# Kernel optimization log

Measured on AMD Instinct MI355X. Metric: run time of the kernel, lower is better.

The kernel has to match this reference:

```python
import jax, jax.numpy as jnp
import numpy as np

B, S, D, HW = 256, 32, 512, 196


def setup_inputs() -> dict:
    key = jax.random.key(0)
    ks = jax.random.split(key, 34)
    n = lambda k, sh, s=1.0: jax.random.normal(k, sh, dtype=jnp.float32) * s
    w = 0.03  # xavier-ish scale for D=512 layers
    return {
        "words": n(ks[0], (B, S, D)),
        "question": n(ks[1], (B, 2 * D)),
        "know": n(ks[2], (B, D, HW)),
        "control0": n(ks[3], (B, D)),
        "memory0": n(ks[4], (B, D)),
        # ControlUnit
        "Wsc": n(ks[5], (2 * D, D), w), "bsc": jnp.zeros((D,), jnp.float32),
        "Wp": n(ks[6], (D, D), w), "bp": jnp.zeros((D,), jnp.float32),
        "Wcq": n(ks[7], (2 * D, D), w), "bcq": jnp.zeros((D,), jnp.float32),
        "wac": n(ks[8], (D, 1), w), "bac": jnp.zeros((1,), jnp.float32),
        # ReadUnit
        "Wm": n(ks[9], (D, D), w), "bm": jnp.zeros((D,), jnp.float32),
        "Wk": n(ks[10], (D, D), w), "bk": jnp.zeros((D,), jnp.float32),
        "Wc1": n(ks[11], (3 * D, D), w), "bc1": jnp.zeros((D,), jnp.float32),
        "Wc2": n(ks[12], (D, D), w), "bc2": jnp.zeros((D,), jnp.float32),
        "war": n(ks[13], (D, 1), w), "bar": jnp.zeros((1,), jnp.float32),
        # WriteUnit (self-attention variant)
        "Wwc": n(ks[14], (D, D), w), "bwc": jnp.zeros((D,), jnp.float32),
        "waw": n(ks[15], (D, 1), w), "baw": jnp.zeros((1,), jnp.float32),
        "Wwcat": n(ks[16], (3 * D, D), w), "bwcat": jnp.zeros((D,), jnp.float32),
    }


def reference(words, question, know, control0, memory0,
              Wsc, bsc, Wp, bp, Wcq, bcq, wac, bac,
              Wm, bm, Wk, bk, Wc1, bc1, Wc2, bc2, war, bar,
              Wwc, bwc, waw, baw, Wwcat, bwcat):
    # ---- ControlUnit (step 0) ----
    q = jnp.tanh(question @ Wsc + bsc)                    # [B,D]
    pa = q @ Wp + bp                                      # position_aware[0]
    cq = jnp.concatenate([control0, pa], axis=1) @ Wcq + bcq  # [B,D]
    logit_c = (cq[:, None, :] * words) @ wac + bac        # [B,S,1]
    attn_c = jax.nn.softmax(logit_c, axis=1)
    control = jnp.sum(attn_c * words, axis=1)             # [B,D]

    # ---- ReadUnit ----
    pm = memory0 @ Wm + bm                                # [B,D]
    pk = jnp.einsum('bdn,de->ben', know, Wk) + bk[None, :, None]  # [B,D,HW]
    pm_b = jnp.broadcast_to(pm[:, :, None], pk.shape)
    feat = jnp.concatenate([pm_b * pk, pk, pm_b], axis=1)  # [B,3D,HW]
    h = jax.nn.relu(jnp.einsum('bfn,fd->bnd', feat, Wc1) + bc1)  # [B,HW,D]
    h = h @ Wc2 + bc2                                     # [B,HW,D]
    logit_r = (h * control[:, None, :]) @ war + bar       # [B,HW,1]
    a_r = jax.nn.softmax(logit_r[..., 0], axis=1)          # [B,HW]
    read = jnp.einsum('bdn,bn->bd', know, a_r)            # [B,D]

    # ---- WriteUnit (self-attention over previous controls; T=1 at step 0) ----
    sc = control @ Wwc + bwc                              # [B,D]
    ctrl_prev = control0[:, :, None]                      # [B,D,T]
    logit_w = jnp.einsum('bdt,d->bt', sc[:, :, None] * ctrl_prev, waw[:, 0]) + baw  # [B,T]
    a_w = jax.nn.softmax(logit_w, axis=1)
    attn_mem = jnp.einsum('bdt,bt->bd', memory0[:, :, None], a_w)  # [B,D]
    concat = jnp.concatenate([read, memory0, attn_mem], axis=1)    # [B,3D]
    next_mem = concat @ Wwcat + bwcat                     # [B,D]

    return control, next_mem
```

## Files before the change

kernel.cpp:

```cpp
#include <hip/hip_runtime.h>
#include <hip/hip_bf16.h>
#include <math.h>

typedef __hip_bfloat16 bf16;
typedef __attribute__((ext_vector_type(8))) short s8v;
typedef __attribute__((ext_vector_type(4))) short s4v;
typedef __attribute__((ext_vector_type(4))) float f4v;

#define BB 256
#define SS 32
#define DD 512
#define HWN 196
#define AP 40

__device__ __forceinline__ float b2f(bf16 x){ return __bfloat162float(x); }
__device__ __forceinline__ bf16 f2b(float x){ return __float2bfloat16(x); }
__device__ __forceinline__ float us2f(unsigned short u){
    union { unsigned int i; float f; } t; t.i = ((unsigned int)u) << 16; return t.f;
}
__device__ __forceinline__ float ldin(int dt, const void* p, size_t i){
    return dt ? b2f(((const bf16*)p)[i]) : ((const float*)p)[i];
}

__global__ void detect_k(const void* q, int* flag){
    __shared__ int cnt;
    if (threadIdx.x == 0) cnt = 0;
    __syncthreads();
    const unsigned short* u = (const unsigned short*)q;
    unsigned short v = u[threadIdx.x * 4];
    int e = (v >> 7) & 0xFF;
    atomicAdd(&cnt, (e >= 100 && e <= 140) ? 1 : 0);
    __syncthreads();
    if (threadIdx.x == 0) *flag = (cnt > 128) ? 1 : 0;
}

struct PJob { const void* s; const void* s_b; const void* s2; const void* s2_b;
              bf16* d; int R, C, ldd, kofs, mode, boff; };
struct PrepP { PJob j[11]; const void* war; const void* bk; float* warf; float* bkf; };

__global__ __launch_bounds__(256) void prep_k(PrepP P, const int* __restrict__ flag){
    const int dt = *flag;
    __shared__ float T[32][33];
    int bx = blockIdx.x;
    int ji = 0;
    #pragma unroll
    for (int i = 0; i < 11; ++i) if (bx >= P.j[i].boff) ji = i;
    PJob jb = P.j[ji];
    const void* src  = dt ? jb.s_b  : jb.s;
    const void* src2 = dt ? jb.s2_b : jb.s2;
    int t = bx - jb.boff;
    int tx = threadIdx.x & 31, ty = threadIdx.x >> 5;
    if (jb.mode == 3){
        for (int i = threadIdx.x; i < DD; i += 256){
            P.warf[i] = ldin(dt, P.war, i);
            P.bkf[i]  = ldin(dt, P.bk, i);
        }
        return;
    }
    int nrt = jb.R >> 5;
    int r0 = (t % nrt) << 5, c0 = (t / nrt) << 5;
    if (jb.mode == 2){
        for (int rr = ty; rr < 32; rr += 8)
            jb.d[(size_t)(r0 + rr) * jb.ldd + jb.kofs + c0 + tx] =
                f2b(ldin(dt, src, (size_t)(r0 + rr) * jb.C + c0 + tx));
        return;
    }
    for (int rr = ty; rr < 32; rr += 8){
        float v = ldin(dt, src, (size_t)(r0 + rr) * jb.C + c0 + tx);
        if (jb.mode == 1) v += ldin(dt, src2, (size_t)(r0 + rr) * jb.C + c0 + tx);
        T[rr][tx] = v;
    }
    __syncthreads();
    for (int rr = ty; rr < 32; rr += 8)
        jb.d[(size_t)(c0 + rr) * jb.ldd + jb.kofs + r0 + tx] = f2b(T[tx][rr]);
}

__device__ __forceinline__ void tile_decode(int idb, int swz, int& rt, int& ct){
    if (swz){ int g = idb >> 6, w = idb & 63; rt = g * 8 + (w & 7); ct = w >> 3; }
    else    { ct = idb & 7; rt = idb >> 3; }
}

__global__ __launch_bounds__(256) void g1_mfma(const void* __restrict__ know,
                                               const bf16* __restrict__ BT,
                                               const float* __restrict__ bkf,
                                               bf16* __restrict__ C,
                                               int b0, int swz,
                                               const int* __restrict__ flag){
    const int dt = *flag;
    __shared__ __align__(16) bf16 As[128 * AP];
    __shared__ __align__(16) bf16 Bs[64 * AP];
    const int tid = threadIdx.x, lane = tid & 63, wave = tid >> 6;
    const int q = lane >> 4, mr = lane & 15;
    int rt, ct; tile_decode(blockIdx.x, swz, rt, ct);
    const int r0 = rt * 128, c0 = ct * 64;
    const int quad = tid >> 3;
    const int kg   = tid & 7;
    const int m    = r0 + quad * 4;
    const int bl   = m / HWN;
    const int n    = m - bl * HWN;
    const size_t abase = ((size_t)(b0 + bl) * DD) * HWN + n;
    f4v acc[2][4];
    #pragma unroll
    for (int t = 0; t < 2; ++t)
        #pragma unroll
        for (int j = 0; j < 4; ++j){ f4v z = {0.f,0.f,0.f,0.f}; acc[t][j] = z; }
    for (int k0 = 0; k0 < DD; k0 += 32){
        union { bf16 h[4]; s4v v; } pk_[4];
        if (dt == 0){
            const float* kp = (const float*)know + abase + (size_t)(k0 + kg * 4) * HWN;
            float4 ra = *(const float4*)kp;
            float4 rb = *(const float4*)(kp + HWN);
            float4 rc = *(const float4*)(kp + 2 * HWN);
            float4 rd4 = *(const float4*)(kp + 3 * HWN);
            #pragma unroll
            for (int j = 0; j < 4; ++j){
                pk_[j].h[0] = f2b((&ra.x)[j]);
                pk_[j].h[1] = f2b((&rb.x)[j]);
                pk_[j].h[2] = f2b((&rc.x)[j]);
                pk_[j].h[3] = f2b((&rd4.x)[j]);
            }
        } else {
            const unsigned short* kp = (const unsigned short*)know + abase + (size_t)(k0 + kg * 4) * HWN;
            ushort4 ua = *(const ushort4*)kp;
            ushort4 ub = *(const ushort4*)(kp + HWN);
            ushort4 uc = *(const ushort4*)(kp + 2 * HWN);
            ushort4 ud = *(const ushort4*)(kp + 3 * HWN);
            #pragma unroll
            for (int j = 0; j < 4; ++j){
                ((unsigned short*)&pk_[j].v)[0] = (&ua.x)[j];
                ((unsigned short*)&pk_[j].v)[1] = (&ub.x)[j];
                ((unsigned short*)&pk_[j].v)[2] = (&uc.x)[j];
                ((unsigned short*)&pk_[j].v)[3] = (&ud.x)[j];
            }
        }
        #pragma unroll
        for (int j = 0; j < 4; ++j)
            *(s4v*)&As[(quad * 4 + j) * AP + kg * 4] = pk_[j].v;
        {
            int col = tid >> 2, ko = (tid & 3) * 8;
            *(float4*)&Bs[col * AP + ko] =
                *(const float4*)(BT + (size_t)(c0 + col) * DD + k0 + ko);
        }
        __syncthreads();
        s8v a0 = *(const s8v*)&As[(wave * 32 + mr) * AP + q * 8];
        s8v a1 = *(const s8v*)&As[(wave * 32 + 16 + mr) * AP + q * 8];
        #pragma unroll
        for (int j = 0; j < 4; ++j){
            s8v b = *(const s8v*)&Bs[(j * 16 + mr) * AP + q * 8];
            acc[0][j] = __builtin_amdgcn_mfma_f32_16x16x32_bf16(a0, b, acc[0][j], 0, 0, 0);
            acc[1][j] = __builtin_amdgcn_mfma_f32_16x16x32_bf16(a1, b, acc[1][j], 0, 0, 0);
        }
        __syncthreads();
    }
    #pragma unroll
    for (int t = 0; t < 2; ++t)
        #pragma unroll
        for (int j = 0; j < 4; ++j)
            #pragma unroll
            for (int i = 0; i < 4; ++i){
                int row = r0 + wave * 32 + t * 16 + q * 4 + i;
                int col = c0 + j * 16 + mr;
                C[(size_t)row * DD + col] = f2b(acc[t][j][i] + bkf[col]);
            }
}

__global__ __launch_bounds__(256) void g2_mfma(const bf16* __restrict__ Apk,
                                               const bf16* __restrict__ BT,
                                               const float* __restrict__ pmf,
                                               const float* __restrict__ t3b,
                                               const float* __restrict__ uf,
                                               float* __restrict__ lpart,
                                               int b0, int swz){
    __shared__ __align__(16) bf16 As[128 * AP];
    __shared__ __align__(16) bf16 Bs[64 * AP];
    const int tid = threadIdx.x, lane = tid & 63, wave = tid >> 6;
    const int q = lane >> 4, mr = lane & 15;
    int idb = blockIdx.x, u, ct;
    if (swz){ int g = idb >> 6, w = idb & 63; u = g * 8 + (w & 7); ct = w >> 3; }
    else    { u = idb >> 3; ct = idb & 7; }
    const int bl = u >> 1, rt = u & 1;
    const int b = b0 + bl;
    const int c0 = ct * 64, rbase = rt * 128;
    const float* pmb = pmf + (size_t)b * DD;
    f4v acc[2][4];
    #pragma unroll
    for (int t = 0; t < 2; ++t)
        #pragma unroll
        for (int j = 0; j < 4; ++j){ f4v z = {0.f,0.f,0.f,0.f}; acc[t][j] = z; }
    for (int k0 = 0; k0 < DD; k0 += 32){
        #pragma unroll
        for (int cc = 0; cc < 2; ++cc){
            int c = tid + cc * 256;
            int row = c >> 2, ko = (c & 3) * 8;
            int rl = rbase + row;
            float4 v = {0.f, 0.f, 0.f, 0.f};
            if (rl < HWN)
                v = *(const float4*)(Apk + ((size_t)bl * HWN + rl) * DD + k0 + ko);
            *(float4*)&As[row * AP + ko] = v;
        }
        {
            int col = tid >> 2, ko = (tid & 3) * 8;
            const bf16* wrow = BT + (size_t)(c0 + col) * (2 * DD) + k0 + ko;
            union { bf16 h[8]; float4 f; } w1, w2, be;
            w1.f = *(const float4*)wrow;
            w2.f = *(const float4*)(wrow + DD);
            float4 pA = *(const float4*)(pmb + k0 + ko);
            float4 pB = *(const float4*)(pmb + k0 + ko + 4);
            #pragma unroll
            for (int j = 0; j < 4; ++j){
                be.h[j]     = f2b((&pA.x)[j] * b2f(w1.h[j])     + b2f(w2.h[j]));
                be.h[4 + j] = f2b((&pB.x)[j] * b2f(w1.h[4 + j]) + b2f(w2.h[4 + j]));
            }
            *(float4*)&Bs[col * AP + ko] = be.f;
        }
        __syncthreads();
        s8v a0 = *(const s8v*)&As[(wave * 32 + mr) * AP + q * 8];
        s8v a1 = *(const s8v*)&As[(wave * 32 + 16 + mr) * AP + q * 8];
        #pragma unroll
        for (int j = 0; j < 4; ++j){
            s8v b2 = *(const s8v*)&Bs[(j * 16 + mr) * AP + q * 8];
            acc[0][j] = __builtin_amdgcn_mfma_f32_16x16x32_bf16(a0, b2, acc[0][j], 0, 0, 0);
            acc[1][j] = __builtin_amdgcn_mfma_f32_16x16x32_bf16(a1, b2, acc[1][j], 0, 0, 0);
        }
        __syncthreads();
    }
    float part[2][4] = {};
    #pragma unroll
    for (int t = 0; t < 2; ++t)
        #pragma unroll
        for (int j = 0; j < 4; ++j)
            #pragma unroll
            for (int i = 0; i < 4; ++i){
                int rl = rbase + wave * 32 + t * 16 + q * 4 + i;
                if (rl < HWN){
                    int col = c0 + j * 16 + mr;
                    float hv = acc[t][j][i] + t3b[(size_t)b * DD + col];
                    part[t][i] += fmaxf(hv, 0.f) * uf[(size_t)b * DD + col];
                }
            }
    #pragma unroll
    for (int t = 0; t < 2; ++t)
        #pragma unroll
        for (int i = 0; i < 4; ++i){
            float v = part[t][i];
            v += __shfl_xor(v, 1, 16);
            v += __shfl_xor(v, 2, 16);
            v += __shfl_xor(v, 4, 16);
            v += __shfl_xor(v, 8, 16);
            int rl = rbase + wave * 32 + t * 16 + q * 4 + i;
            if (mr == 0 && rl < HWN)
                lpart[(size_t)ct * (BB * HWN) + (size_t)b * HWN + rl] = v;
        }
}

struct SSeg { const void* A; int a_ws, lda, K, koff; };
struct SP {
    SSeg s[2]; int nseg;
    const bf16* BT; int ldb;
    const float* amul;
    const void* bias;
    float* C; int M, N, act;
    void* out2; int o2off;
};
struct SPP { SP j[2]; };

__global__ __launch_bounds__(256) void sgemm_k(SPP P, const int* __restrict__ flag){
    const int dt = *flag;
    const SP p = P.j[blockIdx.z];
    const int tid = threadIdx.x, lane = tid & 63, w = tid >> 6;
    const int q = lane >> 4, mr = lane & 15;
    const int n0 = blockIdx.x * 16, m0 = blockIdx.y * 64 + w * 16;
    f4v acc = {0.f,0.f,0.f,0.f};
    for (int sg = 0; sg < p.nseg; ++sg){
        const SSeg s = p.s[sg];
        const float* amul = (sg == 0) ? p.amul : nullptr;
        #pragma unroll 4
        for (int k0 = 0; k0 < s.K; k0 += 32){
            const int kk = k0 + q * 8;
            union { bf16 h[8]; s8v v; } a;
            if (s.a_ws || dt == 0){
                const float* Af = (const float*)s.A + (size_t)(m0 + mr) * s.lda + kk;
                float4 f0 = *(const float4*)Af;
                float4 f1 = *(const float4*)(Af + 4);
                float f[8] = {f0.x, f0.y, f0.z, f0.w, f1.x, f1.y, f1.z, f1.w};
                if (amul){
                    #pragma unroll
                    for (int j = 0; j < 8; ++j) f[j] *= amul[kk + j];
                }
                #pragma unroll
                for (int j = 0; j < 8; ++j) a.h[j] = f2b(f[j]);
            } else {
                a.v = *(const s8v*)((const bf16*)s.A + (size_t)(m0 + mr) * s.lda + kk);
                if (amul){
                    #pragma unroll
                    for (int j = 0; j < 8; ++j) a.h[j] = f2b(b2f(a.h[j]) * amul[kk + j]);
                }
            }
            s8v b = *(const s8v*)(p.BT + (size_t)(n0 + mr) * p.ldb + s.koff + kk);
            acc = __builtin_amdgcn_mfma_f32_16x16x32_bf16(a.v, b, acc, 0, 0, 0);
        }
    }
    #pragma unroll
    for (int i = 0; i < 4; ++i){
        int row = m0 + q * 4 + i, col = n0 + mr;
        float v = acc[i] + (p.bias ? ldin(dt, p.bias, col) : 0.f);
        if (p.act == 1) v = tanhf(v);
        p.C[(size_t)row * p.N + col] = v;
        if (p.out2){
            size_t oi = (size_t)p.o2off + (size_t)row * p.N + col;
            if (dt) ((bf16*)p.out2)[oi] = f2b(v);
            else    ((float*)p.out2)[oi] = v;
        }
    }
}

__global__ __launch_bounds__(256) void attn_control_k(const float* __restrict__ cq,
                                                      const void* __restrict__ wac,
                                                      const void* __restrict__ bac,
                                                      const void* __restrict__ words,
                                                      float* __restrict__ control,
                                                      const void* __restrict__ bc2,
                                                      const float* __restrict__ warf,
                                                      const void* __restrict__ bar,
                                                      float* __restrict__ bias_r,
                                                      void* __restrict__ out,
                                                      const int* __restrict__ flag){
    const int dt = *flag;
    const int b = blockIdx.x, tid = threadIdx.x;
    __shared__ float cw[DD];
    __shared__ float lg[SS];
    __shared__ float es[SS];
    __shared__ float red[256];
    for (int d = tid; d < DD; d += 256) cw[d] = cq[(size_t)b*DD + d] * ldin(dt, wac, d);
    __syncthreads();
    int s = tid >> 3, l8 = tid & 7;
    float p = 0.f;
    for (int d = l8; d < DD; d += 8) p += cw[d] * ldin(dt, words, ((size_t)b*SS + s)*DD + d);
    for (int off = 4; off; off >>= 1) p += __shfl_down(p, off, 8);
    if (l8 == 0) lg[s] = p + ldin(dt, bac, 0);
    __syncthreads();
    if (tid == 0){
        float mx = -INFINITY;
        for (int i = 0; i < SS; ++i) mx = fmaxf(mx, lg[i]);
        float sm = 0.f;
        for (int i = 0; i < SS; ++i){ es[i] = expf(lg[i] - mx); sm += es[i]; }
        float inv = 1.f / sm;
        for (int i = 0; i < SS; ++i) es[i] *= inv;
    }
    __syncthreads();
    float vb = 0.f;
    for (int d = tid; d < DD; d += 256){
        float c = 0.f;
        #pragma unroll 8
        for (int s2 = 0; s2 < SS; ++s2) c += es[s2] * ldin(dt, words, ((size_t)b*SS + s2)*DD + d);
        control[(size_t)b*DD + d] = c;
        if (dt) ((bf16*)out)[(size_t)b*DD + d] = f2b(c);
        else    ((float*)out)[(size_t)b*DD + d] = c;
        vb += ldin(dt, bc2, d) * c * warf[d];
    }
    red[tid] = vb; __syncthreads();
    for (int off = 128; off; off >>= 1){ if (tid < off) red[tid] += red[tid + off]; __syncthreads(); }
    if (tid == 0) bias_r[b] = red[0] + ldin(dt, bar, 0);
}

__global__ __launch_bounds__(256) void softmax_read_k(const float* __restrict__ lpart,
                                                      const float* __restrict__ bias_r,
                                                      const void* __restrict__ know,
                                                      float* __restrict__ readout,
                                                      const int* __restrict__ flag){
    const int dt = *flag;
    const int b = blockIdx.x, tid = threadIdx.x;
    __shared__ float a[HWN];
    __shared__ float red[256];
    float x = -INFINITY;
    if (tid < HWN){
        float sacc = bias_r[b];
        #pragma unroll
        for (int c = 0; c < 8; ++c)
            sacc += lpart[(size_t)c * (BB * HWN) + (size_t)b * HWN + tid];
        x = sacc;
    }
    red[tid] = x; __syncthreads();
    for (int off = 128; off; off >>= 1){ if (tid < off) red[tid] = fmaxf(red[tid], red[tid + off]); __syncthreads(); }
    float mx = red[0]; __syncthreads();
    float e = (tid < HWN) ? expf(x - mx) : 0.f;
    red[tid] = e; __syncthreads();
    for (int off = 128; off; off >>= 1){ if (tid < off) red[tid] += red[tid + off]; __syncthreads(); }
    float inv = 1.f / red[0];
    if (tid < HWN) a[tid] = e * inv;
    __syncthreads();
    for (int d = tid; d < DD; d += 256){
        size_t base = ((size_t)b*DD + d) * HWN;
        float sum = 0.f;
        if (dt){
            const ushort4* k4 = (const ushort4*)((const unsigned short*)know + base);
            #pragma unroll 7
            for (int c = 0; c < HWN/4; ++c){
                ushort4 u4 = k4[c];
                sum += a[4*c+0]*us2f(u4.x) + a[4*c+1]*us2f(u4.y)
                     + a[4*c+2]*us2f(u4.z) + a[4*c+3]*us2f(u4.w);
            }
        } else {
            const float4* k4 = (const float4*)((const float*)know + base);
            #pragma unroll 7
            for (int c = 0; c < HWN/4; ++c){
                float4 f4 = k4[c];
                sum += a[4*c+0]*f4.x + a[4*c+1]*f4.y + a[4*c+2]*f4.z + a[4*c+3]*f4.w;
            }
        }
        readout[(size_t)b*DD + d] = sum;
    }
}

extern "C" void kernel_launch(void* const* d_in, const int* in_sizes, int n_in,
                              void* d_out, int out_size, void* d_ws, size_t ws_size,
                              hipStream_t stream){
    const void* words    = d_in[0];
    const void* question = d_in[1];
    const void* know     = d_in[2];
    const void* control0 = d_in[3];
    const void* memory0  = d_in[4];
    const void* Wsc = d_in[5];   const void* bsc = d_in[6];
    const void* Wp  = d_in[7];   const void* bp  = d_in[8];
    const void* Wcq = d_in[9];   const void* bcq = d_in[10];
    const void* wac = d_in[11];  const void* bac = d_in[12];
    const void* Wm  = d_in[13];  const void* bm  = d_in[14];
    const void* Wk  = d_in[15];  const void* bk  = d_in[16];
    const void* Wc1 = d_in[17];  const void* bc1 = d_in[18];
    const void* Wc2 = d_in[19];  const void* bc2 = d_in[20];
    const void* war = d_in[21];  const void* bar = d_in[22];
    const void* Wwcat = d_in[27]; const void* bwcat = d_in[28];

    int* flag = (int*)d_ws;
    float* F = ((float*)d_ws) + 16;
    const int NBD = BB * DD;
    float* q_   = F;
    float* pa   = F + 1*NBD;
    float* cq   = F + 2*NBD;
    float* ctrl = F + 3*NBD;
    float* pm   = F + 4*NBD;
    float* t3b  = F + 5*NBD;
    float* u_   = F + 6*NBD;
    float* rd   = F + 7*NBD;
    float* nm   = F + 8*NBD;
    float* bias_r = F + 9*NBD;
    float* warf   = bias_r + BB;
    float* bkf    = warf + DD;
    float* lpart  = bkf + DD;
    size_t off_f = 16 + 9*(size_t)NBD + BB + 2*DD + 8*(size_t)BB*HWN;
    size_t byte_off = (off_f * 4 + 255) & ~(size_t)255;
    bf16* WB = (bf16*)((char*)d_ws + byte_off);
    bf16* WscT   = WB;
    bf16* WcqT   = WscT  + (size_t)DD*2*DD;
    bf16* Wc1T2  = WcqT  + (size_t)DD*2*DD;
    bf16* WwcatF = Wc1T2 + (size_t)DD*2*DD;
    bf16* WpT    = WwcatF+ (size_t)DD*2*DD;
    bf16* WmT    = WpT   + (size_t)DD*DD;
    bf16* Wc1t3T = WmT   + (size_t)DD*DD;
    bf16* WkT    = Wc1t3T+ (size_t)DD*DD;
    bf16* Wc2cv  = WkT   + (size_t)DD*DD;
    size_t big_off = (byte_off + ((size_t)DD*2*DD*4 + (size_t)DD*DD*5) * sizeof(bf16) + 255) & ~(size_t)255;

    size_t per_batch = (size_t)HWN * DD * sizeof(bf16);
    size_t avail = (ws_size > big_off) ? (ws_size - big_off) : 0;
    int CB = (int)(avail / per_batch);
    CB &= ~31;
    if (CB > BB) CB = BB;
    if (CB < 32) CB = 32;
    bf16* pkT = (bf16*)((char*)d_ws + big_off);

    dim3 blk(256);

    detect_k<<<dim3(1), blk, 0, stream>>>(question, flag);

    {
        PrepP P; int bo = 0;
        auto J = [&](const void* s, const void* sb, const void* s2, const void* s2b,
                     bf16* d, int R, int C, int ldd, int kofs, int mode, int idx){
            int nb = (mode == 3) ? 1 : ((R >> 5) * (C >> 5));
            P.j[idx] = PJob{ s, sb, s2, s2b, d, R, C, ldd, kofs, mode, bo };
            bo += nb;
        };
        const void* Wc1t3_f = (const void*)((const float*)Wc1 + (size_t)2*DD*DD);
        const void* Wc1t3_b = (const void*)((const bf16*) Wc1 + (size_t)2*DD*DD);
        const void* Ww1_f = (const void*)((const float*)Wwcat + (size_t)DD*DD);
        const void* Ww1_b = (const void*)((const bf16*) Wwcat + (size_t)DD*DD);
        const void* Ww2_f = (const void*)((const float*)Wwcat + (size_t)2*DD*DD);
        const void* Ww2_b = (const void*)((const bf16*) Wwcat + (size_t)2*DD*DD);
        J(Wsc,   Wsc,   nullptr, nullptr, WscT,   2*DD, DD, 2*DD, 0,   0, 0);
        J(Wp,    Wp,    nullptr, nullptr, WpT,    DD,   DD, DD,   0,   0, 1);
        J(Wcq,   Wcq,   nullptr, nullptr, WcqT,   2*DD, DD, 2*DD, 0,   0, 2);
        J(Wm,    Wm,    nullptr, nullptr, WmT,    DD,   DD, DD,   0,   0, 3);
        J(Wc1,   Wc1,   nullptr, nullptr, Wc1T2,  2*DD, DD, 2*DD, 0,   0, 4);
        J(Wc1t3_f, Wc1t3_b, nullptr, nullptr, Wc1t3T, DD, DD, DD, 0,   0, 5);
        J(Wk,    Wk,    nullptr, nullptr, WkT,    DD,   DD, DD,   0,   0, 6);
        J(Wwcat, Wwcat, nullptr, nullptr, WwcatF, DD,   DD, 2*DD, 0,   0, 7);
        J(Ww1_f, Ww1_b, Ww2_f,   Ww2_b,   WwcatF, DD,   DD, 2*DD, 512, 1, 8);
        J(Wc2,   Wc2,   nullptr, nullptr, Wc2cv,  DD,   DD, DD,   0,   2, 9);
        J(nullptr,nullptr,nullptr,nullptr,nullptr,0,    0,  0,    0,   3, 10);
        P.war = war; P.bk = bk; P.warf = warf; P.bkf = bkf;
        prep_k<<<dim3(bo), blk, 0, stream>>>(P, flag);
    }

    SPP P2;
    auto mkjob = [&](SP& p){ p = SP{}; };

    mkjob(P2.j[0]);
    P2.j[0].nseg = 1;
    P2.j[0].s[0] = SSeg{ question, 0, 2*DD, 2*DD, 0 };
    P2.j[0].BT = WscT; P2.j[0].ldb = 2*DD;
    P2.j[0].bias = bsc; P2.j[0].C = q_; P2.j[0].M = BB; P2.j[0].N = DD; P2.j[0].act = 1;
    mkjob(P2.j[1]);
    P2.j[1].nseg = 1;
    P2.j[1].s[0] = SSeg{ memory0, 0, DD, DD, 0 };
    P2.j[1].BT = WmT; P2.j[1].ldb = DD;
    P2.j[1].bias = bm; P2.j[1].C = pm; P2.j[1].M = BB; P2.j[1].N = DD; P2.j[1].act = 0;
    sgemm_k<<<dim3(DD/16, BB/64, 2), blk, 0, stream>>>(P2, flag);

    mkjob(P2.j[0]);
    P2.j[0].nseg = 1;
    P2.j[0].s[0] = SSeg{ q_, 1, DD, DD, 0 };
    P2.j[0].BT = WpT; P2.j[0].ldb = DD;
    P2.j[0].bias = bp; P2.j[0].C = pa; P2.j[0].M = BB; P2.j[0].N = DD; P2.j[0].act = 0;
    mkjob(P2.j[1]);
    P2.j[1].nseg = 1;
    P2.j[1].s[0] = SSeg{ pm, 1, DD, DD, 0 };
    P2.j[1].BT = Wc1t3T; P2.j[1].ldb = DD;
    P2.j[1].bias = bc1; P2.j[1].C = t3b; P2.j[1].M = BB; P2.j[1].N = DD; P2.j[1].act = 0;
    sgemm_k<<<dim3(DD/16, BB/64, 2), blk, 0, stream>>>(P2, flag);

    mkjob(P2.j[0]);
    P2.j[0].nseg = 2;
    P2.j[0].s[0] = SSeg{ control0, 0, DD, DD, 0 };
    P2.j[0].s[1] = SSeg{ pa,       1, DD, DD, 512 };
    P2.j[0].BT = WcqT; P2.j[0].ldb = 2*DD;
    P2.j[0].bias = bcq; P2.j[0].C = cq; P2.j[0].M = BB; P2.j[0].N = DD; P2.j[0].act = 0;
    sgemm_k<<<dim3(DD/16, BB/64, 1), blk, 0, stream>>>(P2, flag);

    attn_control_k<<<dim3(BB), blk, 0, stream>>>(cq, wac, bac, words, ctrl,
                                                 bc2, warf, bar, bias_r, d_out, flag);

    mkjob(P2.j[0]);
    P2.j[0].nseg = 1;
    P2.j[0].s[0] = SSeg{ ctrl, 1, DD, DD, 0 };
    P2.j[0].BT = Wc2cv; P2.j[0].ldb = DD; P2.j[0].amul = warf;
    P2.j[0].C = u_; P2.j[0].M = BB; P2.j[0].N = DD; P2.j[0].act = 0;
    sgemm_k<<<dim3(DD/16, BB/64, 1), blk, 0, stream>>>(P2, flag);

    for (int b0 = 0; b0 < BB; b0 += CB){
        int cb = (b0 + CB <= BB) ? CB : (BB - b0);
        int M = cb * HWN;
        int nR = M / 128;
        int swz1 = (nR % 8 == 0) ? 1 : 0;
        g1_mfma<<<dim3(8 * nR), blk, 0, stream>>>(know, WkT, bkf, pkT, b0, swz1, flag);
        int nU = cb * 2;
        int swz2 = (nU % 8 == 0) ? 1 : 0;
        g2_mfma<<<dim3(8 * nU), blk, 0, stream>>>(pkT, Wc1T2, pm, t3b, u_, lpart, b0, swz2);
    }

    softmax_read_k<<<dim3(BB), blk, 0, stream>>>(lpart, bias_r, know, rd, flag);

    mkjob(P2.j[0]);
    P2.j[0].nseg = 2;
    P2.j[0].s[0] = SSeg{ rd,      1, DD, DD, 0 };
    P2.j[0].s[1] = SSeg{ memory0, 0, DD, DD, 512 };
    P2.j[0].BT = WwcatF; P2.j[0].ldb = 2*DD;
    P2.j[0].bias = bwcat; P2.j[0].C = nm; P2.j[0].M = BB; P2.j[0].N = DD; P2.j[0].act = 0;
    P2.j[0].out2 = d_out; P2.j[0].o2off = NBD;
    sgemm_k<<<dim3(DD/16, BB/64, 1), blk, 0, stream>>>(P2, flag);
}
```

Measured before the change: 561.4 us.

## Enlarge MFMA GEMM tiles to 128x128 with 64-wide K steps

Both MFMA GEMM kernels (know projection and the Wc1 stage) move from 128x64 output tiles with 32-wide K steps to 128x128 tiles with 64-wide K steps. Each wave now holds twice as many accumulators. The grid is halved, the block swizzle decode is adjusted, and the logit partial count read by the softmax is cut from 8 column tiles to 4. This is meant to reuse each A tile across more output columns, cut global and LDS traffic per FLOP, and halve the barriers per K. The cost is more registers and LDS per block, which may lower occupancy, and fewer blocks in flight.

```diff
diff --git a/kernel.cpp b/kernel.cpp
--- a/kernel.cpp
+++ b/kernel.cpp
@@ -11,7 +11,7 @@
 #define SS 32
 #define DD 512
 #define HWN 196
-#define AP 40
+#define APW 72
 
 __device__ __forceinline__ float b2f(bf16 x){ return __bfloat162float(x); }
 __device__ __forceinline__ bf16 f2b(float x){ return __float2bfloat16(x); }
@@ -75,11 +75,6 @@
         jb.d[(size_t)(c0 + rr) * jb.ldd + jb.kofs + r0 + tx] = f2b(T[tx][rr]);
 }
 
-__device__ __forceinline__ void tile_decode(int idb, int swz, int& rt, int& ct){
-    if (swz){ int g = idb >> 6, w = idb & 63; rt = g * 8 + (w & 7); ct = w >> 3; }
-    else    { ct = idb & 7; rt = idb >> 3; }
-}
-
 __global__ __launch_bounds__(256) void g1_mfma(const void* __restrict__ know,
                                                const bf16* __restrict__ BT,
                                                const float* __restrict__ bkf,
@@ -87,81 +82,95 @@
                                                int b0, int swz,
                                                const int* __restrict__ flag){
     const int dt = *flag;
-    __shared__ __align__(16) bf16 As[128 * AP];
-    __shared__ __align__(16) bf16 Bs[64 * AP];
+    __shared__ __align__(16) bf16 As[128 * APW];
+    __shared__ __align__(16) bf16 Bs[128 * APW];
     const int tid = threadIdx.x, lane = tid & 63, wave = tid >> 6;
     const int q = lane >> 4, mr = lane & 15;
-    int rt, ct; tile_decode(blockIdx.x, swz, rt, ct);
-    const int r0 = rt * 128, c0 = ct * 64;
+    int idb = blockIdx.x, rt, ct;
+    if (swz){ int g = idb >> 5, w = idb & 31; rt = g * 8 + (w & 7); ct = w >> 3; }
+    else    { rt = idb >> 2; ct = idb & 3; }
+    const int r0 = rt * 128, c0 = ct * 128;
     const int quad = tid >> 3;
     const int kg   = tid & 7;
     const int m    = r0 + quad * 4;
     const int bl   = m / HWN;
     const int n    = m - bl * HWN;
     const size_t abase = ((size_t)(b0 + bl) * DD) * HWN + n;
-    f4v acc[2][4];
+    f4v acc[2][8];
     #pragma unroll
     for (int t = 0; t < 2; ++t)
         #pragma unroll
-        for (int j = 0; j < 4; ++j){ f4v z = {0.f,0.f,0.f,0.f}; acc[t][j] = z; }
-    for (int k0 = 0; k0 < DD; k0 += 32){
-        union { bf16 h[4]; s4v v; } pk_[4];
-        if (dt == 0){
-            const float* kp = (const float*)know + abase + (size_t)(k0 + kg * 4) * HWN;
-            float4 ra = *(const float4*)kp;
-            float4 rb = *(const float4*)(kp + HWN);
-            float4 rc = *(const float4*)(kp + 2 * HWN);
-            float4 rd4 = *(const float4*)(kp + 3 * HWN);
-            #pragma unroll
-            for (int j = 0; j < 4; ++j){
-                pk_[j].h[0] = f2b((&ra.x)[j]);
-                pk_[j].h[1] = f2b((&rb.x)[j]);
-                pk_[j].h[2] = f2b((&rc.x)[j]);
-                pk_[j].h[3] = f2b((&rd4.x)[j]);
-            }
-        } else {
-            const unsigned short* kp = (const unsigned short*)know + abase + (size_t)(k0 + kg * 4) * HWN;
-            ushort4 ua = *(const ushort4*)kp;
-            ushort4 ub = *(const ushort4*)(kp + HWN);
-            ushort4 uc = *(const ushort4*)(kp + 2 * HWN);
-            ushort4 ud = *(const ushort4*)(kp + 3 * HWN);
-            #pragma unroll
-            for (int j = 0; j < 4; ++j){
-                ((unsigned short*)&pk_[j].v)[0] = (&ua.x)[j];
-                ((unsigned short*)&pk_[j].v)[1] = (&ub.x)[j];
-                ((unsigned short*)&pk_[j].v)[2] = (&uc.x)[j];
-                ((unsigned short*)&pk_[j].v)[3] = (&ud.x)[j];
-            }
-        }
-        #pragma unroll
-        for (int j = 0; j < 4; ++j)
-            *(s4v*)&As[(quad * 4 + j) * AP + kg * 4] = pk_[j].v;
+        for (int j = 0; j < 8; ++j){ f4v z = {0.f,0.f,0.f,0.f}; acc[t][j] = z; }
+    for (int k0 = 0; k0 < DD; k0 += 64){
+        #pragma unroll
+        for (int h = 0; h < 2; ++h){
+            int kb = k0 + h * 32 + kg * 4;
+            union { bf16 hh[4]; s4v v; } pk_[4];
+            if (dt == 0){
+                const float* kp = (const float*)know + abase + (size_t)kb * HWN;
+                float4 ra  = *(const float4*)kp;
+                float4 rb  = *(const float4*)(kp + HWN);
+                float4 rc  = *(const float4*)(kp + 2 * HWN);
+                float4 rd4 = *(const float4*)(kp + 3 * HWN);
+                #pragma unroll
+                for (int j = 0; j < 4; ++j){
+                    pk_[j].hh[0] = f2b((&ra.x)[j]);
+                    pk_[j].hh[1] = f2b((&rb.x)[j]);
+                    pk_[j].hh[2] = f2b((&rc.x)[j]);
+                    pk_[j].hh[3] = f2b((&rd4.x)[j]);
+                }
+            } else {
+                const unsigned short* kp = (const unsigned short*)know + abase + (size_t)kb * HWN;
+                ushort4 ua = *(const ushort4*)kp;
+                ushort4 ub = *(const ushort4*)(kp + HWN);
+                ushort4 uc = *(const ushort4*)(kp + 2 * HWN);
+                ushort4 ud = *(const ushort4*)(kp + 3 * HWN);
+                #pragma unroll
+                for (int j = 0; j < 4; ++j){
+                    ((unsigned short*)&pk_[j].v)[0] = (&ua.x)[j];
+                    ((unsigned short*)&pk_[j].v)[1] = (&ub.x)[j];
+                    ((unsigned short*)&pk_[j].v)[2] = (&uc.x)[j];
+                    ((unsigned short*)&pk_[j].v)[3] = (&ud.x)[j];
+                }
+            }
+            #pragma unroll
+            for (int j = 0; j < 4; ++j)
+                *(s4v*)&As[(quad * 4 + j) * APW + h * 32 + kg * 4] = pk_[j].v;
+        }
         {
-            int col = tid >> 2, ko = (tid & 3) * 8;
-            *(float4*)&Bs[col * AP + ko] =
-                *(const float4*)(BT + (size_t)(c0 + col) * DD + k0 + ko);
+            int col = tid >> 1, kb = (tid & 1) * 32;
+            const bf16* wp = BT + (size_t)(c0 + col) * DD + k0 + kb;
+            bf16* dst = &Bs[col * APW + kb];
+            #pragma unroll
+            for (int t4 = 0; t4 < 32; t4 += 8)
+                *(float4*)(dst + t4) = *(const float4*)(wp + t4);
         }
         __syncthreads();
-        s8v a0 = *(const s8v*)&As[(wave * 32 + mr) * AP + q * 8];
-        s8v a1 = *(const s8v*)&As[(wave * 32 + 16 + mr) * AP + q * 8];
-        #pragma unroll
-        for (int j = 0; j < 4; ++j){
-            s8v b = *(const s8v*)&Bs[(j * 16 + mr) * AP + q * 8];
-            acc[0][j] = __builtin_amdgcn_mfma_f32_16x16x32_bf16(a0, b, acc[0][j], 0, 0, 0);
-            acc[1][j] = __builtin_amdgcn_mfma_f32_16x16x32_bf16(a1, b, acc[1][j], 0, 0, 0);
+        #pragma unroll
+        for (int h = 0; h < 2; ++h){
+            s8v a0 = *(const s8v*)&As[(wave * 32 + mr) * APW + h * 32 + q * 8];
+            s8v a1 = *(const s8v*)&As[(wave * 32 + 16 + mr) * APW + h * 32 + q * 8];
+            #pragma unroll
+            for (int j = 0; j < 8; ++j){
+                s8v b = *(const s8v*)&Bs[(j * 16 + mr) * APW + h * 32 + q * 8];
+                acc[0][j] = __builtin_amdgcn_mfma_f32_16x16x32_bf16(a0, b, acc[0][j], 0, 0, 0);
+                acc[1][j] = __builtin_amdgcn_mfma_f32_16x16x32_bf16(a1, b, acc[1][j], 0, 0, 0);
+            }
         }
         __syncthreads();
     }
     #pragma unroll
     for (int t = 0; t < 2; ++t)
         #pragma unroll
-        for (int j = 0; j < 4; ++j)
+        for (int j = 0; j < 8; ++j){
+            float bb = bkf[c0 + j * 16 + mr];
             #pragma unroll
             for (int i = 0; i < 4; ++i){
                 int row = r0 + wave * 32 + t * 16 + q * 4 + i;
                 int col = c0 + j * 16 + mr;
-                C[(size_t)row * DD + col] = f2b(acc[t][j][i] + bkf[col]);
-            }
+                C[(size_t)row * DD + col] = f2b(acc[t][j][i] + bb);
+            }
+        }
 }
 
 __global__ __launch_bounds__(256) void g2_mfma(const bf16* __restrict__ Apk,
@@ -171,56 +180,69 @@
                                                const float* __restrict__ uf,
                                                float* __restrict__ lpart,
                                                int b0, int swz){
-    __shared__ __align__(16) bf16 As[128 * AP];
-    __shared__ __align__(16) bf16 Bs[64 * AP];
+    __shared__ __align__(16) bf16 As[128 * APW];
+    __shared__ __align__(16) bf16 Bs[128 * APW];
     const int tid = threadIdx.x, lane = tid & 63, wave = tid >> 6;
     const int q = lane >> 4, mr = lane & 15;
     int idb = blockIdx.x, u, ct;
-    if (swz){ int g = idb >> 6, w = idb & 63; u = g * 8 + (w & 7); ct = w >> 3; }
-    else    { u = idb >> 3; ct = idb & 7; }
+    if (swz){ int g = idb >> 5, w = idb & 31; u = g * 8 + (w & 7); ct = w >> 3; }
+    else    { u = idb >> 2; ct = idb & 3; }
     const int bl = u >> 1, rt = u & 1;
     const int b = b0 + bl;
-    const int c0 = ct * 64, rbase = rt * 128;
+    const int c0 = ct * 128, rbase = rt * 128;
     const float* pmb = pmf + (size_t)b * DD;
-    f4v acc[2][4];
+    f4v acc[2][8];
     #pragma unroll
     for (int t = 0; t < 2; ++t)
         #pragma unroll
-        for (int j = 0; j < 4; ++j){ f4v z = {0.f,0.f,0.f,0.f}; acc[t][j] = z; }
-    for (int k0 = 0; k0 < DD; k0 += 32){
-        #pragma unroll
-        for (int cc = 0; cc < 2; ++cc){
-            int c = tid + cc * 256;
-            int row = c >> 2, ko = (c & 3) * 8;
+        for (int j = 0; j < 8; ++j){ f4v z = {0.f,0.f,0.f,0.f}; acc[t][j] = z; }
+    for (int k0 = 0; k0 < DD; k0 += 64){
+        {
+            int row = tid >> 1, kb = (tid & 1) * 32;
             int rl = rbase + row;
-            float4 v = {0.f, 0.f, 0.f, 0.f};
-            if (rl < HWN)
-                v = *(const float4*)(Apk + ((size_t)bl * HWN + rl) * DD + k0 + ko);
-            *(float4*)&As[row * AP + ko] = v;
+            bf16* dst = &As[row * APW + kb];
+            if (rl < HWN){
+                const bf16* ap = Apk + ((size_t)bl * HWN + rl) * DD + k0 + kb;
+                #pragma unroll
+                for (int t4 = 0; t4 < 32; t4 += 8)
+                    *(float4*)(dst + t4) = *(const float4*)(ap + t4);
+            } else {
+                float4 z = {0.f,0.f,0.f,0.f};
+                #pragma unroll
+                for (int t4 = 0; t4 < 32; t4 += 8)
+                    *(float4*)(dst + t4) = z;
+            }
         }
         {
-            int col = tid >> 2, ko = (tid & 3) * 8;
-            const bf16* wrow = BT + (size_t)(c0 + col) * (2 * DD) + k0 + ko;
-            union { bf16 h[8]; float4 f; } w1, w2, be;
-            w1.f = *(const float4*)wrow;
-            w2.f = *(const float4*)(wrow + DD);
-            float4 pA = *(const float4*)(pmb + k0 + ko);
-            float4 pB = *(const float4*)(pmb + k0 + ko + 4);
-            #pragma unroll
-            for (int j = 0; j < 4; ++j){
-                be.h[j]     = f2b((&pA.x)[j] * b2f(w1.h[j])     + b2f(w2.h[j]));
-                be.h[4 + j] = f2b((&pB.x)[j] * b2f(w1.h[4 + j]) + b2f(w2.h[4 + j]));
-            }
-            *(float4*)&Bs[col * AP + ko] = be.f;
+            int col = tid >> 1, kb = (tid & 1) * 32;
+            const bf16* wrow = BT + (size_t)(c0 + col) * (2 * DD) + k0 + kb;
+            bf16* dst = &Bs[col * APW + kb];
+            #pragma unroll
+            for (int t4 = 0; t4 < 32; t4 += 8){
+                union { bf16 h[8]; float4 f; } w1, w2, be;
+                w1.f = *(const float4*)(wrow + t4);
+                w2.f = *(const float4*)(wrow + DD + t4);
+                float4 pA = *(const float4*)(pmb + k0 + kb + t4);
+                float4 pB = *(const float4*)(pmb + k0 + kb + t4 + 4);
+                #pragma unroll
+                for (int j = 0; j < 4; ++j){
+                    be.h[j]     = f2b((&pA.x)[j] * b2f(w1.h[j])     + b2f(w2.h[j]));
+                    be.h[4 + j] = f2b((&pB.x)[j] * b2f(w1.h[4 + j]) + b2f(w2.h[4 + j]));
+                }
+                *(float4*)(dst + t4) = be.f;
+            }
         }
         __syncthreads();
-        s8v a0 = *(const s8v*)&As[(wave * 32 + mr) * AP + q * 8];
-        s8v a1 = *(const s8v*)&As[(wave * 32 + 16 + mr) * AP + q * 8];
-        #pragma unroll
-        for (int j = 0; j < 4; ++j){
-            s8v b2 = *(const s8v*)&Bs[(j * 16 + mr) * AP + q * 8];
-            acc[0][j] = __builtin_amdgcn_mfma_f32_16x16x32_bf16(a0, b2, acc[0][j], 0, 0, 0);
-            acc[1][j] = __builtin_amdgcn_mfma_f32_16x16x32_bf16(a1, b2, acc[1][j], 0, 0, 0);
+        #pragma unroll
+        for (int h = 0; h < 2; ++h){
+            s8v a0 = *(const s8v*)&As[(wave * 32 + mr) * APW + h * 32 + q * 8];
+            s8v a1 = *(const s8v*)&As[(wave * 32 + 16 + mr) * APW + h * 32 + q * 8];
+            #pragma unroll
+            for (int j = 0; j < 8; ++j){
+                s8v b2 = *(const s8v*)&Bs[(j * 16 + mr) * APW + h * 32 + q * 8];
+                acc[0][j] = __builtin_amdgcn_mfma_f32_16x16x32_bf16(a0, b2, acc[0][j], 0, 0, 0);
+                acc[1][j] = __builtin_amdgcn_mfma_f32_16x16x32_bf16(a1, b2, acc[1][j], 0, 0, 0);
+            }
         }
         __syncthreads();
     }
@@ -228,7 +250,7 @@
     #pragma unroll
     for (int t = 0; t < 2; ++t)
         #pragma unroll
-        for (int j = 0; j < 4; ++j)
+        for (int j = 0; j < 8; ++j)
             #pragma unroll
             for (int i = 0; i < 4; ++i){
                 int rl = rbase + wave * 32 + t * 16 + q * 4 + i;
@@ -376,7 +398,7 @@
     if (tid < HWN){
         float sacc = bias_r[b];
         #pragma unroll
-        for (int c = 0; c < 8; ++c)
+        for (int c = 0; c < 4; ++c)
             sacc += lpart[(size_t)c * (BB * HWN) + (size_t)b * HWN + tid];
         x = sacc;
     }
@@ -552,10 +574,10 @@
         int M = cb * HWN;
         int nR = M / 128;
         int swz1 = (nR % 8 == 0) ? 1 : 0;
-        g1_mfma<<<dim3(8 * nR), blk, 0, stream>>>(know, WkT, bkf, pkT, b0, swz1, flag);
+        g1_mfma<<<dim3(4 * nR), blk, 0, stream>>>(know, WkT, bkf, pkT, b0, swz1, flag);
         int nU = cb * 2;
         int swz2 = (nU % 8 == 0) ? 1 : 0;
-        g2_mfma<<<dim3(8 * nU), blk, 0, stream>>>(pkT, Wc1T2, pm, t3b, u_, lpart, b0, swz2);
+        g2_mfma<<<dim3(4 * nU), blk, 0, stream>>>(pkT, Wc1T2, pm, t3b, u_, lpart, b0, swz2);
     }
 
     softmax_read_k<<<dim3(BB), blk, 0, stream>>>(lpart, bias_r, know, rd, flag);
```

New measurement: 556.8 us. About the same (-0.8%).
